# Optimization experiments

Hardware: AMD Instinct MI355X
Metric: run time of the kernel (lower is better)

Reference implementation:

```python
import jax, jax.numpy as jnp
import numpy as np

B, S, HID = 1, 2048, 2048
NH, NKV, D = 32, 4, 128   # query heads, kv heads, head_dim
ROPE_THETA = 1e6
EPS = 1e-6


def _rms_norm(x, w):
    # per-head RMSNorm over head_dim, computed in fp32 (Qwen3MoeRMSNorm)
    xf = x.astype(jnp.float32)
    var = jnp.mean(xf * xf, axis=-1, keepdims=True)
    return (w * (xf * jax.lax.rsqrt(var + EPS))).astype(x.dtype)


def _rotate_half(x):
    x1, x2 = jnp.split(x, 2, axis=-1)
    return jnp.concatenate([-x2, x1], axis=-1)


def setup_inputs() -> dict:
    key = jax.random.key(0)
    ks = jax.random.split(key, 5)
    hidden_states = jax.random.normal(ks[0], (B, S, HID), jnp.float32)
    # weights stored as (in, out); torch Linear computes x @ W.T with W (out,in) -- same math
    wq = jax.random.normal(ks[1], (HID, NH * D), jnp.float32) * 0.02
    wk = jax.random.normal(ks[2], (HID, NKV * D), jnp.float32) * 0.02
    wv = jax.random.normal(ks[3], (HID, NKV * D), jnp.float32) * 0.02
    wo = jax.random.normal(ks[4], (NH * D, HID), jnp.float32) * 0.02
    q_norm_w = jnp.ones((D,), jnp.float32)
    k_norm_w = jnp.ones((D,), jnp.float32)
    # RoPE tables (rotate_half convention, like HF Qwen3)
    inv_freq = 1.0 / (ROPE_THETA ** (jnp.arange(0, D, 2, dtype=jnp.float32) / D))
    freqs = jnp.arange(S, dtype=jnp.float32)[:, None] * inv_freq[None, :]  # [S, D/2]
    emb = jnp.concatenate([freqs, freqs], axis=-1)  # [S, D]
    cos, sin = jnp.cos(emb), jnp.sin(emb)
    # causal mask (True = keep)
    attention_mask = jnp.tril(jnp.ones((S, S), bool))[None, None]
    return {
        'hidden_states': hidden_states, 'cos': cos, 'sin': sin,
        'wq': wq, 'wk': wk, 'wv': wv, 'wo': wo,
        'q_norm_w': q_norm_w, 'k_norm_w': k_norm_w,
        'attention_mask': attention_mask, 'start_pos': 0,
    }


def reference(hidden_states, cos, sin, wq, wk, wv, wo, q_norm_w, k_norm_w,
              attention_mask, start_pos):
    b, s, _ = hidden_states.shape
    # projections + per-head RMSNorm, then [B, H, S, D]
    q = _rms_norm((hidden_states @ wq).reshape(b, s, NH, D), q_norm_w).transpose(0, 2, 1, 3)
    k = _rms_norm((hidden_states @ wk).reshape(b, s, NKV, D), k_norm_w).transpose(0, 2, 1, 3)
    v = (hidden_states @ wv).reshape(b, s, NKV, D).transpose(0, 2, 1, 3)
    # rotary embedding (rotate_half form); start_pos=0 -> tables already aligned
    c = cos[None, None, :, :]
    sn = sin[None, None, :, :]
    q = q * c + _rotate_half(q) * sn
    k = k * c + _rotate_half(k) * sn
    # GQA: repeat kv heads to match query heads
    groups = NH // NKV
    k = jnp.repeat(k, groups, axis=1)
    v = jnp.repeat(v, groups, axis=1)
    scaling = D ** -0.5
    scores = jnp.einsum('bhqd,bhkd->bhqk', q, k) * scaling  # [B, NH, S, S]
    scores = jnp.where(attention_mask, scores, jnp.float32(-1e9))
    attn = jax.nn.softmax(scores, axis=-1)
    out = jnp.einsum('bhqk,bhkd->bhqd', attn, v)  # [B, NH, S, D]
    out = out.transpose(0, 2, 1, 3).reshape(b, s, NH * D)
    return out @ wo
```

## Files before the change

### kernel.cpp

```cpp
#include <hip/hip_runtime.h>
#include <hip/hip_bf16.h>

using short4v = __attribute__((ext_vector_type(4))) short;
using short8 = __attribute__((ext_vector_type(8))) short;
using f32x4  = __attribute__((ext_vector_type(4))) float;

#define SEQ 2048
#define NHEAD 32
#define NKVH 4
#define HDIM 128
#define QK_SCALE_LOG2 (0.08838834764831845f * 1.44269504088896340f)

__device__ __forceinline__ float fast_exp2(float x) { return __builtin_amdgcn_exp2f(x); }
__device__ __forceinline__ float b2f(short u) {
    return __uint_as_float(((unsigned)(unsigned short)u) << 16);
}
__device__ __forceinline__ short f2bb(float f) {
    __hip_bfloat16 h = __float2bfloat16(f);
    return *reinterpret_cast<short*>(&h);
}

__global__ __launch_bounds__(256) void prep_kernel(
    const float* __restrict__ hs, __hip_bfloat16* __restrict__ hsb,
    const float* __restrict__ wq, const float* __restrict__ wk, const float* __restrict__ wv,
    const float* __restrict__ wo,
    __hip_bfloat16* __restrict__ WqkvT, __hip_bfloat16* __restrict__ WoT) {
    const int b = blockIdx.x, tid = threadIdx.x;
    if (b < 4096) {
        int i = b * 256 + tid;
        float4 v = ((const float4*)hs)[i];
        __hip_bfloat16 h4[4] = {__float2bfloat16(v.x), __float2bfloat16(v.y),
                                __float2bfloat16(v.z), __float2bfloat16(v.w)};
        ((ushort4*)hsb)[i] = *(ushort4*)h4;
        return;
    }
    __shared__ float tile[32][33];
    const float* W; __hip_bfloat16* Wt; int N, ld, nb, kb;
    if (b < 12288)      { int bb = b - 4096;  W = wq; Wt = WqkvT;                       N = 4096; ld = 2048; nb = (bb & 127) * 32; kb = (bb >> 7) * 32; }
    else if (b < 13312) { int bb = b - 12288; W = wk; Wt = WqkvT + (size_t)4096 * 2048; N = 512;  ld = 2048; nb = (bb & 15) * 32;  kb = (bb >> 4) * 32; }
    else if (b < 14336) { int bb = b - 13312; W = wv; Wt = WqkvT + (size_t)4608 * 2048; N = 512;  ld = 2048; nb = (bb & 15) * 32;  kb = (bb >> 4) * 32; }
    else                { int bb = b - 14336; W = wo; Wt = WoT;                         N = 2048; ld = 4096; nb = (bb & 63) * 32;  kb = (bb >> 6) * 32; }
    int tx = tid & 31, ty = tid >> 5;
    for (int j = 0; j < 32; j += 8)
        tile[ty + j][tx] = W[(size_t)(kb + ty + j) * N + nb + tx];
    __syncthreads();
    for (int j = 0; j < 32; j += 8)
        Wt[(size_t)(nb + ty + j) * ld + kb + tx] = __float2bfloat16(tile[tx][ty + j]);
}

__global__ void add2b_kernel(const __hip_bfloat16* __restrict__ a, const __hip_bfloat16* __restrict__ b,
                             float* __restrict__ o, int n4) {
    int i = blockIdx.x * blockDim.x + threadIdx.x;
    if (i >= n4) return;
    short4v x = ((const short4v*)a)[i];
    short4v y = ((const short4v*)b)[i];
    float4 z = {b2f(x[0]) + b2f(y[0]), b2f(x[1]) + b2f(y[1]),
                b2f(x[2]) + b2f(y[2]), b2f(x[3]) + b2f(y[3])};
    ((float4*)o)[i] = z;
}

#define BM 128
#define BN 128
#define BKK 32
template <typename OutT>
__global__ __launch_bounds__(256) void gemm_bt_kernel(
    const __hip_bfloat16* __restrict__ A, const __hip_bfloat16* __restrict__ Bt,
    OutT* __restrict__ C, int M, int N, int Kext, int ld, int koff, long long czstride) {
    A  += (size_t)blockIdx.z * koff;
    Bt += (size_t)blockIdx.z * koff;
    C  += (size_t)blockIdx.z * czstride;
    __shared__ __align__(16) __hip_bfloat16 sA[BM * BKK];
    __shared__ __align__(16) __hip_bfloat16 sB[BN * BKK];
    const int tid = threadIdx.x;
    const int w = tid >> 6, l = tid & 63;
    const int wr = w >> 1, wc = w & 1;
    const int row0 = blockIdx.y * BM;
    const int col0 = blockIdx.x * BN;
    const int srow = l >> 2;
    const int scol = (l & 3) * 8;

    f32x4 acc[4][4] = {};
    const int fr = l & 15;
    const int fc = (l >> 4) * 8;

    for (int k0 = 0; k0 < Kext; k0 += BKK) {
        for (int i = 0; i < 2; ++i) {
            int c = i * 4 + w;
            const __hip_bfloat16* ga = A + (size_t)(row0 + c * 16 + srow) * ld + k0 + scol;
            __builtin_amdgcn_global_load_lds((const __attribute__((address_space(1))) void*)ga,
                                             (__attribute__((address_space(3))) void*)&sA[c * 16 * BKK], 16, 0, 0);
            const __hip_bfloat16* gb = Bt + (size_t)(col0 + c * 16 + srow) * ld + k0 + scol;
            __builtin_amdgcn_global_load_lds((const __attribute__((address_space(1))) void*)gb,
                                             (__attribute__((address_space(3))) void*)&sB[c * 16 * BKK], 16, 0, 0);
        }
        __syncthreads();
        short8 af[4], bfr[4];
        for (int m = 0; m < 4; ++m)
            af[m] = *(const short8*)&sA[(wr * 64 + m * 16 + fr) * BKK + fc];
        for (int n = 0; n < 4; ++n)
            bfr[n] = *(const short8*)&sB[(wc * 64 + n * 16 + fr) * BKK + fc];
        for (int m = 0; m < 4; ++m)
            for (int n = 0; n < 4; ++n)
                acc[m][n] = __builtin_amdgcn_mfma_f32_16x16x32_bf16(af[m], bfr[n], acc[m][n], 0, 0, 0);
        __syncthreads();
    }
    const int fq = l >> 4;
    for (int m = 0; m < 4; ++m)
        for (int n = 0; n < 4; ++n)
            for (int r = 0; r < 4; ++r) {
                int row = row0 + wr * 64 + m * 16 + fq * 4 + r;
                int col = col0 + wc * 64 + n * 16 + fr;
                float v = acc[m][n][r];
                if constexpr (__is_same(OutT, float)) C[(size_t)row * N + col] = v;
                else C[(size_t)row * N + col] = __float2bfloat16(v);
            }
}

__global__ __launch_bounds__(256) void pack_kernel(
    const __hip_bfloat16* __restrict__ P0, const __hip_bfloat16* __restrict__ P1,
    const float* __restrict__ cosp, const float* __restrict__ sinp,
    const float* __restrict__ qnw, const float* __restrict__ knw,
    __hip_bfloat16* __restrict__ Qh, __hip_bfloat16* __restrict__ Kh, __hip_bfloat16* __restrict__ Vt) {
    const int tid = threadIdx.x;
    const int rloc = tid >> 4, l16 = tid & 15;
    const int r = blockIdx.y * 16 + rloc;
    const int s = blockIdx.x * 2 + (r >= 40 ? 1 : 0);
    const int slot = (r >= 40) ? r - 40 : r;
    int off;
    if (slot < 32)      off = slot * 128;
    else if (slot < 36) off = 4096 + (slot - 32) * 128;
    else                off = 4608 + (slot - 36) * 128;
    const int d0 = l16 * 4;
    const size_t base = (size_t)s * 5120 + off;

    short4v a0 = *(const short4v*)&P0[base + d0];
    short4v a1 = *(const short4v*)&P0[base + d0 + 64];
    short4v b0 = *(const short4v*)&P1[base + d0];
    short4v b1 = *(const short4v*)&P1[base + d0 + 64];
    float x1[4], x2[4];
    for (int j = 0; j < 4; ++j) {
        x1[j] = b2f(a0[j]) + b2f(b0[j]);
        x2[j] = b2f(a1[j]) + b2f(b1[j]);
    }

    if (slot >= 36) {
        int t = slot - 36;
        for (int j = 0; j < 4; ++j) {
            Vt[((size_t)t * 128 + d0 + j) * SEQ + s]      = __float2bfloat16(x1[j]);
            Vt[((size_t)t * 128 + d0 + 64 + j) * SEQ + s] = __float2bfloat16(x2[j]);
        }
        return;
    }
    float ss = 0.f;
    for (int j = 0; j < 4; ++j) ss += x1[j] * x1[j] + x2[j] * x2[j];
    for (int x = 1; x < 16; x <<= 1) ss += __shfl_xor(ss, x);
    float rs = rsqrtf(ss * (1.0f / 128.0f) + 1e-6f);

    f32x4 c4 = *(const f32x4*)&cosp[(size_t)s * 128 + d0];
    f32x4 s4 = *(const f32x4*)&sinp[(size_t)s * 128 + d0];
    const float* wgt = (slot < 32) ? qnw : knw;
    f32x4 w1 = *(const f32x4*)&wgt[d0];
    f32x4 w2 = *(const f32x4*)&wgt[d0 + 64];
    const float scl = (slot < 32) ? QK_SCALE_LOG2 : 1.0f;

    short4v o1, o2;
    for (int j = 0; j < 4; ++j) {
        float a = x1[j] * rs * w1[j], b = x2[j] * rs * w2[j];
        o1[j] = f2bb((a * c4[j] - b * s4[j]) * scl);
        o2[j] = f2bb((b * c4[j] + a * s4[j]) * scl);
    }
    __hip_bfloat16* dst;
    if (slot < 32) dst = Qh + ((size_t)slot * SEQ + s) * 128;
    else           dst = Kh + ((size_t)(slot - 32) * SEQ + s) * 128;
    *(short4v*)&dst[d0]      = o1;
    *(short4v*)&dst[d0 + 64] = o2;
}

__global__ __launch_bounds__(256, 2) void attn_kernel(
    const __hip_bfloat16* __restrict__ Qh,
    const __hip_bfloat16* __restrict__ Kh,
    const __hip_bfloat16* __restrict__ Vt,
    __hip_bfloat16* __restrict__ Oa) {
    __shared__ __align__(16) __hip_bfloat16 sK[2][64 * 128];
    __shared__ __align__(16) __hip_bfloat16 sV[2][128 * 64];
    __shared__ __align__(16) __hip_bfloat16 sP[4][16 * 72];

    const int tid = threadIdx.x;
    const int w = tid >> 6, l = tid & 63;
    const int bx = blockIdx.x;
    const int y = bx & 7;
    const int qt = 127 - (bx >> 3);
    const int qbase = qt * 16;
    const int hkv = y >> 1;
    const int h = y * 4 + w;
    const int fr = l & 15, g = l >> 4;

    const __hip_bfloat16* Qp = Qh + ((size_t)h * SEQ + qbase) * HDIM;
    const __hip_bfloat16* Kp = Kh + (size_t)hkv * SEQ * HDIM;
    const __hip_bfloat16* Vp = Vt + (size_t)hkv * HDIM * SEQ;
    __hip_bfloat16* myP = &sP[w][0];

    short8 qf[4];
    for (int c = 0; c < 4; ++c)
        qf[c] = *(const short8*)&Qp[fr * HDIM + c * 32 + g * 8];

    f32x4 oacc[8] = {};
    float mrow[4], lpart[4];
    for (int r = 0; r < 4; ++r) { mrow[r] = -3.0e38f; lpart[r] = 0.f; }

    const int xr = (fr & 7) << 4;
    const int ntiles = ((qbase + 15) >> 6) + 1;

    auto stage = [&](int buf, int kbase) {
        for (int i = 0; i < 4; ++i) {
            int blk = i * 4 + w;
            {
                int row = blk * 4 + (l >> 4);
                int cb = ((l & 15) * 16) ^ ((row & 7) << 4);
                const __hip_bfloat16* src = Kp + (size_t)(kbase + row) * HDIM + (cb >> 1);
                __builtin_amdgcn_global_load_lds((const __attribute__((address_space(1))) void*)src,
                    (__attribute__((address_space(3))) void*)&sK[buf][blk * 512], 16, 0, 0);
            }
            {
                int row = blk * 8 + (l >> 3);
                int cb = ((l & 7) * 16) ^ ((row & 7) << 4);
                const __hip_bfloat16* src = Vp + (size_t)row * SEQ + kbase + (cb >> 1);
                __builtin_amdgcn_global_load_lds((const __attribute__((address_space(1))) void*)src,
                    (__attribute__((address_space(3))) void*)&sV[buf][blk * 512], 16, 0, 0);
            }
        }
    };

    stage(0, 0);
    __syncthreads();

    for (int t = 0; t < ntiles; ++t) {
        const int kbase = t * 64;
        const int buf = t & 1;
        if (t + 1 < ntiles) stage(buf ^ 1, kbase + 64);

        f32x4 s[4] = {};
        __builtin_amdgcn_s_setprio(1);
        for (int j = 0; j < 4; ++j) {
            const __hip_bfloat16* kp = &sK[buf][(j * 16 + fr) * 128];
            for (int c = 0; c < 4; ++c) {
                short8 kf = *(const short8*)&kp[((c * 64 + g * 16) ^ xr) >> 1];
                s[j] = __builtin_amdgcn_mfma_f32_16x16x32_bf16(qf[c], kf, s[j], 0, 0, 0);
            }
        }
        __builtin_amdgcn_s_setprio(0);
        float v[4][4], mloc[4];
        const bool full = (kbase + 63 <= qbase);
        for (int r = 0; r < 4; ++r) {
            if (full) {
                v[r][0] = s[0][r]; v[r][1] = s[1][r]; v[r][2] = s[2][r]; v[r][3] = s[3][r];
            } else {
                const int qg = qbase + g * 4 + r;
                v[r][0] = (kbase + fr      <= qg) ? s[0][r] : -1e30f;
                v[r][1] = (kbase + 16 + fr <= qg) ? s[1][r] : -1e30f;
                v[r][2] = (kbase + 32 + fr <= qg) ? s[2][r] : -1e30f;
                v[r][3] = (kbase + 48 + fr <= qg) ? s[3][r] : -1e30f;
            }
            float m = fmaxf(fmaxf(v[r][0], v[r][1]), fmaxf(v[r][2], v[r][3]));
            for (int x = 1; x < 16; x <<= 1) m = fmaxf(m, __shfl_xor(m, x));
            mloc[r] = m;
        }
        int grow = (mloc[0] > mrow[0] + 12.0f) | (mloc[1] > mrow[1] + 12.0f) |
                   (mloc[2] > mrow[2] + 12.0f) | (mloc[3] > mrow[3] + 12.0f);
        if (__any(grow)) {
            for (int r = 0; r < 4; ++r) {
                float mnew = fmaxf(mrow[r], mloc[r]);
                float corr = fast_exp2(mrow[r] - mnew);
                mrow[r] = mnew;
                lpart[r] *= corr;
                for (int dt = 0; dt < 8; ++dt) oacc[dt][r] *= corr;
            }
        }
        for (int r = 0; r < 4; ++r) {
            float e0 = fast_exp2(v[r][0] - mrow[r]);
            float e1 = fast_exp2(v[r][1] - mrow[r]);
            float e2 = fast_exp2(v[r][2] - mrow[r]);
            float e3 = fast_exp2(v[r][3] - mrow[r]);
            lpart[r] += (e0 + e1) + (e2 + e3);
            const int prow = (g * 4 + r) * 72;
            myP[prow + fr]      = __float2bfloat16(e0);
            myP[prow + 16 + fr] = __float2bfloat16(e1);
            myP[prow + 32 + fr] = __float2bfloat16(e2);
            myP[prow + 48 + fr] = __float2bfloat16(e3);
        }
        short8 pa0 = *(const short8*)&myP[fr * 72 + g * 8];
        short8 pa1 = *(const short8*)&myP[fr * 72 + 32 + g * 8];
        __builtin_amdgcn_s_setprio(1);
        for (int dt = 0; dt < 8; ++dt) {
            const __hip_bfloat16* vp = &sV[buf][(dt * 16 + fr) * 64];
            short8 vb0 = *(const short8*)&vp[((g * 16)      ^ xr) >> 1];
            short8 vb1 = *(const short8*)&vp[((g * 16 + 64) ^ xr) >> 1];
            oacc[dt] = __builtin_amdgcn_mfma_f32_16x16x32_bf16(pa0, vb0, oacc[dt], 0, 0, 0);
            oacc[dt] = __builtin_amdgcn_mfma_f32_16x16x32_bf16(pa1, vb1, oacc[dt], 0, 0, 0);
        }
        __builtin_amdgcn_s_setprio(0);
        __syncthreads();
    }

    float inv[4];
    for (int r = 0; r < 4; ++r) {
        float lsum = lpart[r];
        for (int x = 1; x < 16; x <<= 1) lsum += __shfl_xor(lsum, x);
        inv[r] = 1.0f / lsum;
    }
    for (int dt = 0; dt < 8; ++dt)
        for (int r = 0; r < 4; ++r) {
            int qg = qbase + g * 4 + r;
            Oa[(size_t)qg * (NHEAD * HDIM) + h * HDIM + dt * 16 + fr] =
                __float2bfloat16(oacc[dt][r] * inv[r]);
        }
}

extern "C" void kernel_launch(void* const* d_in, const int* in_sizes, int n_in,
                              void* d_out, int out_size, void* d_ws, size_t ws_size,
                              hipStream_t stream) {
    const float* hs   = (const float*)d_in[0];
    const float* cosp = (const float*)d_in[1];
    const float* sinp = (const float*)d_in[2];
    const float* wq   = (const float*)d_in[3];
    const float* wk   = (const float*)d_in[4];
    const float* wv   = (const float*)d_in[5];
    const float* wo   = (const float*)d_in[6];
    const float* qnw  = (const float*)d_in[7];
    const float* knw  = (const float*)d_in[8];
    float* out = (float*)d_out;
    char* ws = (char*)d_ws;

    __hip_bfloat16* hsb    = (__hip_bfloat16*)(ws);
    __hip_bfloat16* WqkvT  = (__hip_bfloat16*)(ws + 8388608);
    __hip_bfloat16* WoT    = (__hip_bfloat16*)(ws + 29360128);
    __hip_bfloat16* P0     = (__hip_bfloat16*)(ws + 46137344);
    __hip_bfloat16* P1     = (__hip_bfloat16*)(ws + 67108864);
    __hip_bfloat16* Qh     = (__hip_bfloat16*)(ws + 8388608);
    __hip_bfloat16* Kh     = (__hip_bfloat16*)(ws + 25165824);
    __hip_bfloat16* Vt     = (__hip_bfloat16*)(ws + 27262976);
    __hip_bfloat16* Oa     = (__hip_bfloat16*)(ws + 46137344);
    __hip_bfloat16* Qb0    = (__hip_bfloat16*)(ws + 67108864);
    __hip_bfloat16* Qb1    = (__hip_bfloat16*)(ws + 75497472);

    prep_kernel<<<22528, 256, 0, stream>>>(hs, hsb, wq, wk, wv, wo, WqkvT, WoT);
    gemm_bt_kernel<__hip_bfloat16><<<dim3(40, 16, 2), 256, 0, stream>>>(
        hsb, WqkvT, P0, 2048, 5120, 1024, 2048, 1024, 10485760LL);
    pack_kernel<<<dim3(1024, 5), 256, 0, stream>>>(P0, P1, cosp, sinp, qnw, knw, Qh, Kh, Vt);
    attn_kernel<<<dim3(1024), 256, 0, stream>>>(Qh, Kh, Vt, Oa);
    gemm_bt_kernel<__hip_bfloat16><<<dim3(16, 16, 2), 256, 0, stream>>>(
        Oa, WoT, Qb0, 2048, 2048, 2048, 4096, 2048, 4194304LL);
    add2b_kernel<<<4096, 256, 0, stream>>>(Qb0, Qb1, out, (2048 * 2048) / 4);
}
```

Measured before the change: 245.0 us.

## Single-buffer attention KV via register prefetch and use 3-way split-K output GEMM

Attention now prefetches the next K/V tile into registers and writes it into a single LDS buffer after compute, replacing double-buffered direct-to-LDS loads. This halves K/V LDS use so occupancy can rise to 3 blocks per CU, at the cost of extra registers and a second barrier per tile. The output projection is split over three K chunks instead of two to give more blocks, with a 3-way add kernel to reduce the partial sums.

New measurement: 262.0 us. 7.0% more time.

```diff
diff --git a/kernel.cpp b/kernel.cpp
--- a/kernel.cpp
+++ b/kernel.cpp
@@ -48,15 +48,16 @@
         Wt[(size_t)(nb + ty + j) * ld + kb + tx] = __float2bfloat16(tile[tx][ty + j]);
 }
 
-__global__ void add2b_kernel(const __hip_bfloat16* __restrict__ a, const __hip_bfloat16* __restrict__ b,
-                             float* __restrict__ o, int n4) {
+__global__ void add3b_kernel(const __hip_bfloat16* __restrict__ a, const __hip_bfloat16* __restrict__ b,
+                             const __hip_bfloat16* __restrict__ c, float* __restrict__ o, int n4) {
     int i = blockIdx.x * blockDim.x + threadIdx.x;
     if (i >= n4) return;
     short4v x = ((const short4v*)a)[i];
     short4v y = ((const short4v*)b)[i];
-    float4 z = {b2f(x[0]) + b2f(y[0]), b2f(x[1]) + b2f(y[1]),
-                b2f(x[2]) + b2f(y[2]), b2f(x[3]) + b2f(y[3])};
-    ((float4*)o)[i] = z;
+    short4v z = ((const short4v*)c)[i];
+    float4 r = {b2f(x[0]) + b2f(y[0]) + b2f(z[0]), b2f(x[1]) + b2f(y[1]) + b2f(z[1]),
+                b2f(x[2]) + b2f(y[2]) + b2f(z[2]), b2f(x[3]) + b2f(y[3]) + b2f(z[3])};
+    ((float4*)o)[i] = r;
 }
 
 #define BM 128
@@ -65,9 +66,11 @@
 template <typename OutT>
 __global__ __launch_bounds__(256) void gemm_bt_kernel(
     const __hip_bfloat16* __restrict__ A, const __hip_bfloat16* __restrict__ Bt,
-    OutT* __restrict__ C, int M, int N, int Kext, int ld, int koff, long long czstride) {
-    A  += (size_t)blockIdx.z * koff;
-    Bt += (size_t)blockIdx.z * koff;
+    OutT* __restrict__ C, int M, int N, int KextMax, int ld, int koff, long long czstride, int Ktot) {
+    const int kstart = blockIdx.z * koff;
+    const int Kext = min(KextMax, Ktot - kstart);
+    A  += (size_t)kstart;
+    Bt += (size_t)kstart;
     C  += (size_t)blockIdx.z * czstride;
     __shared__ __align__(16) __hip_bfloat16 sA[BM * BKK];
     __shared__ __align__(16) __hip_bfloat16 sB[BN * BKK];
@@ -176,13 +179,13 @@
     *(short4v*)&dst[d0 + 64] = o2;
 }
 
-__global__ __launch_bounds__(256, 2) void attn_kernel(
+__global__ __launch_bounds__(256, 3) void attn_kernel(
     const __hip_bfloat16* __restrict__ Qh,
     const __hip_bfloat16* __restrict__ Kh,
     const __hip_bfloat16* __restrict__ Vt,
     __hip_bfloat16* __restrict__ Oa) {
-    __shared__ __align__(16) __hip_bfloat16 sK[2][64 * 128];
-    __shared__ __align__(16) __hip_bfloat16 sV[2][128 * 64];
+    __shared__ __align__(16) __hip_bfloat16 sK[64 * 128];
+    __shared__ __align__(16) __hip_bfloat16 sV[128 * 64];
     __shared__ __align__(16) __hip_bfloat16 sP[4][16 * 72];
 
     const int tid = threadIdx.x;
@@ -211,38 +214,39 @@
     const int xr = (fr & 7) << 4;
     const int ntiles = ((qbase + 15) >> 6) + 1;
 
-    auto stage = [&](int buf, int kbase) {
+    f32x4 kreg[4], vreg[4];
+    auto loadKV = [&](int kbase) {
         for (int i = 0; i < 4; ++i) {
-            int blk = i * 4 + w;
-            {
-                int row = blk * 4 + (l >> 4);
-                int cb = ((l & 15) * 16) ^ ((row & 7) << 4);
-                const __hip_bfloat16* src = Kp + (size_t)(kbase + row) * HDIM + (cb >> 1);
-                __builtin_amdgcn_global_load_lds((const __attribute__((address_space(1))) void*)src,
-                    (__attribute__((address_space(3))) void*)&sK[buf][blk * 512], 16, 0, 0);
-            }
-            {
-                int row = blk * 8 + (l >> 3);
-                int cb = ((l & 7) * 16) ^ ((row & 7) << 4);
-                const __hip_bfloat16* src = Vp + (size_t)row * SEQ + kbase + (cb >> 1);
-                __builtin_amdgcn_global_load_lds((const __attribute__((address_space(1))) void*)src,
-                    (__attribute__((address_space(3))) void*)&sV[buf][blk * 512], 16, 0, 0);
-            }
+            int ch = i * 256 + tid;
+            int rk = ch >> 4, ck = ch & 15;
+            kreg[i] = *(const f32x4*)&Kp[(size_t)(kbase + rk) * HDIM + ck * 8];
+            int rv = ch >> 3, cv = ch & 7;
+            vreg[i] = *(const f32x4*)&Vp[(size_t)rv * SEQ + kbase + cv * 8];
         }
     };
-
-    stage(0, 0);
+    auto writeKV = [&]() {
+        for (int i = 0; i < 4; ++i) {
+            int ch = i * 256 + tid;
+            int rk = ch >> 4, ck = ch & 15;
+            *(f32x4*)((char*)sK + rk * 256 + ((ck * 16) ^ ((rk & 7) << 4))) = kreg[i];
+            int rv = ch >> 3, cv = ch & 7;
+            *(f32x4*)((char*)sV + rv * 128 + ((cv * 16) ^ ((rv & 7) << 4))) = vreg[i];
+        }
+    };
+
+    loadKV(0);
+    writeKV();
     __syncthreads();
 
     for (int t = 0; t < ntiles; ++t) {
         const int kbase = t * 64;
-        const int buf = t & 1;
-        if (t + 1 < ntiles) stage(buf ^ 1, kbase + 64);
+        const bool more = (t + 1 < ntiles);
+        if (more) loadKV(kbase + 64);
 
         f32x4 s[4] = {};
         __builtin_amdgcn_s_setprio(1);
         for (int j = 0; j < 4; ++j) {
-            const __hip_bfloat16* kp = &sK[buf][(j * 16 + fr) * 128];
+            const __hip_bfloat16* kp = &sK[(j * 16 + fr) * 128];
             for (int c = 0; c < 4; ++c) {
                 short8 kf = *(const short8*)&kp[((c * 64 + g * 16) ^ xr) >> 1];
                 s[j] = __builtin_amdgcn_mfma_f32_16x16x32_bf16(qf[c], kf, s[j], 0, 0, 0);
@@ -292,7 +296,7 @@
         short8 pa1 = *(const short8*)&myP[fr * 72 + 32 + g * 8];
         __builtin_amdgcn_s_setprio(1);
         for (int dt = 0; dt < 8; ++dt) {
-            const __hip_bfloat16* vp = &sV[buf][(dt * 16 + fr) * 64];
+            const __hip_bfloat16* vp = &sV[(dt * 16 + fr) * 64];
             short8 vb0 = *(const short8*)&vp[((g * 16)      ^ xr) >> 1];
             short8 vb1 = *(const short8*)&vp[((g * 16 + 64) ^ xr) >> 1];
             oacc[dt] = __builtin_amdgcn_mfma_f32_16x16x32_bf16(pa0, vb0, oacc[dt], 0, 0, 0);
@@ -300,6 +304,10 @@
         }
         __builtin_amdgcn_s_setprio(0);
         __syncthreads();
+        if (more) {
+            writeKV();
+            __syncthreads();
+        }
     }
 
     float inv[4];
@@ -340,15 +348,14 @@
     __hip_bfloat16* Kh     = (__hip_bfloat16*)(ws + 25165824);
     __hip_bfloat16* Vt     = (__hip_bfloat16*)(ws + 27262976);
     __hip_bfloat16* Oa     = (__hip_bfloat16*)(ws + 46137344);
-    __hip_bfloat16* Qb0    = (__hip_bfloat16*)(ws + 67108864);
-    __hip_bfloat16* Qb1    = (__hip_bfloat16*)(ws + 75497472);
+    __hip_bfloat16* Qb     = (__hip_bfloat16*)(ws);
 
     prep_kernel<<<22528, 256, 0, stream>>>(hs, hsb, wq, wk, wv, wo, WqkvT, WoT);
     gemm_bt_kernel<__hip_bfloat16><<<dim3(40, 16, 2), 256, 0, stream>>>(
-        hsb, WqkvT, P0, 2048, 5120, 1024, 2048, 1024, 10485760LL);
+        hsb, WqkvT, P0, 2048, 5120, 1024, 2048, 1024, 10485760LL, 2048);
     pack_kernel<<<dim3(1024, 5), 256, 0, stream>>>(P0, P1, cosp, sinp, qnw, knw, Qh, Kh, Vt);
     attn_kernel<<<dim3(1024), 256, 0, stream>>>(Qh, Kh, Vt, Oa);
-    gemm_bt_kernel<__hip_bfloat16><<<dim3(16, 16, 2), 256, 0, stream>>>(
-        Oa, WoT, Qb0, 2048, 2048, 2048, 4096, 2048, 4194304LL);
-    add2b_kernel<<<4096, 256, 0, stream>>>(Qb0, Qb1, out, (2048 * 2048) / 4);
-}
+    gemm_bt_kernel<__hip_bfloat16><<<dim3(16, 16, 3), 256, 0, stream>>>(
+        Oa, WoT, Qb, 2048, 2048, 1376, 4096, 1376, 4194304LL, 4096);
+    add3b_kernel<<<4096, 256, 0, stream>>>(Qb, Qb + 4194304, Qb + 8388608, out, (2048 * 2048) / 4);
+}
```

## Pair causal query tiles per attention block and split Wo GEMM K three ways

Applied to the files above, without the earlier changes.

The attention kernel now processes two query tiles per block, a short one (qt) and its mirror (127-qt), sharing the staged K/V tiles so each block does balanced causal work and K/V loads are reused. The grid halves to 512 blocks, and register use roughly doubles for the accumulators. The output projection GEMM switches from a 2-way to a 3-way split-K with a ragged final chunk, and a new 3-input add kernel reduces the partials. This adds more parallel blocks for the GEMM at the cost of extra partial traffic.

Measured after the change: 241.2 us. About the same (-1.5%).

```diff
diff --git a/kernel.cpp b/kernel.cpp
--- a/kernel.cpp
+++ b/kernel.cpp
@@ -48,15 +48,16 @@
         Wt[(size_t)(nb + ty + j) * ld + kb + tx] = __float2bfloat16(tile[tx][ty + j]);
 }
 
-__global__ void add2b_kernel(const __hip_bfloat16* __restrict__ a, const __hip_bfloat16* __restrict__ b,
-                             float* __restrict__ o, int n4) {
+__global__ void add3b_kernel(const __hip_bfloat16* __restrict__ a, const __hip_bfloat16* __restrict__ b,
+                             const __hip_bfloat16* __restrict__ c, float* __restrict__ o, int n4) {
     int i = blockIdx.x * blockDim.x + threadIdx.x;
     if (i >= n4) return;
     short4v x = ((const short4v*)a)[i];
     short4v y = ((const short4v*)b)[i];
-    float4 z = {b2f(x[0]) + b2f(y[0]), b2f(x[1]) + b2f(y[1]),
-                b2f(x[2]) + b2f(y[2]), b2f(x[3]) + b2f(y[3])};
-    ((float4*)o)[i] = z;
+    short4v z = ((const short4v*)c)[i];
+    float4 r = {b2f(x[0]) + b2f(y[0]) + b2f(z[0]), b2f(x[1]) + b2f(y[1]) + b2f(z[1]),
+                b2f(x[2]) + b2f(y[2]) + b2f(z[2]), b2f(x[3]) + b2f(y[3]) + b2f(z[3])};
+    ((float4*)o)[i] = r;
 }
 
 #define BM 128
@@ -65,9 +66,11 @@
 template <typename OutT>
 __global__ __launch_bounds__(256) void gemm_bt_kernel(
     const __hip_bfloat16* __restrict__ A, const __hip_bfloat16* __restrict__ Bt,
-    OutT* __restrict__ C, int M, int N, int Kext, int ld, int koff, long long czstride) {
-    A  += (size_t)blockIdx.z * koff;
-    Bt += (size_t)blockIdx.z * koff;
+    OutT* __restrict__ C, int M, int N, int KextMax, int ld, int koff, long long czstride, int Ktot) {
+    const int kstart = blockIdx.z * koff;
+    const int Kext = min(KextMax, Ktot - kstart);
+    A  += (size_t)kstart;
+    Bt += (size_t)kstart;
     C  += (size_t)blockIdx.z * czstride;
     __shared__ __align__(16) __hip_bfloat16 sA[BM * BKK];
     __shared__ __align__(16) __hip_bfloat16 sB[BN * BKK];
@@ -189,27 +192,37 @@
     const int w = tid >> 6, l = tid & 63;
     const int bx = blockIdx.x;
     const int y = bx & 7;
-    const int qt = 127 - (bx >> 3);
-    const int qbase = qt * 16;
+    const int qtA = bx >> 3;
+    const int qbaseA = qtA * 16;
+    const int qbaseB = (127 - qtA) * 16;
     const int hkv = y >> 1;
     const int h = y * 4 + w;
     const int fr = l & 15, g = l >> 4;
 
-    const __hip_bfloat16* Qp = Qh + ((size_t)h * SEQ + qbase) * HDIM;
     const __hip_bfloat16* Kp = Kh + (size_t)hkv * SEQ * HDIM;
     const __hip_bfloat16* Vp = Vt + (size_t)hkv * HDIM * SEQ;
     __hip_bfloat16* myP = &sP[w][0];
 
-    short8 qf[4];
-    for (int c = 0; c < 4; ++c)
-        qf[c] = *(const short8*)&Qp[fr * HDIM + c * 32 + g * 8];
-
-    f32x4 oacc[8] = {};
-    float mrow[4], lpart[4];
-    for (int r = 0; r < 4; ++r) { mrow[r] = -3.0e38f; lpart[r] = 0.f; }
+    short8 qfA[4], qfB[4];
+    {
+        const __hip_bfloat16* QpA = Qh + ((size_t)h * SEQ + qbaseA) * HDIM;
+        const __hip_bfloat16* QpB = Qh + ((size_t)h * SEQ + qbaseB) * HDIM;
+        for (int c = 0; c < 4; ++c) {
+            qfA[c] = *(const short8*)&QpA[fr * HDIM + c * 32 + g * 8];
+            qfB[c] = *(const short8*)&QpB[fr * HDIM + c * 32 + g * 8];
+        }
+    }
+
+    f32x4 oaccA[8] = {}, oaccB[8] = {};
+    float mrowA[4], lpartA[4], mrowB[4], lpartB[4];
+    for (int r = 0; r < 4; ++r) {
+        mrowA[r] = -3.0e38f; lpartA[r] = 0.f;
+        mrowB[r] = -3.0e38f; lpartB[r] = 0.f;
+    }
 
     const int xr = (fr & 7) << 4;
-    const int ntiles = ((qbase + 15) >> 6) + 1;
+    const int nA = ((qbaseA + 15) >> 6) + 1;
+    const int nB = ((qbaseB + 15) >> 6) + 1;
 
     auto stage = [&](int buf, int kbase) {
         for (int i = 0; i < 4; ++i) {
@@ -231,88 +244,100 @@
         }
     };
 
+#define PROCESS(QF, OACC, MROW, LPART, QBASE)                                          \
+    {                                                                                  \
+        f32x4 s[4] = {};                                                               \
+        __builtin_amdgcn_s_setprio(1);                                                 \
+        for (int j = 0; j < 4; ++j) {                                                  \
+            const __hip_bfloat16* kp = &sK[buf][(j * 16 + fr) * 128];                  \
+            for (int c = 0; c < 4; ++c) {                                              \
+                short8 kf = *(const short8*)&kp[((c * 64 + g * 16) ^ xr) >> 1];        \
+                s[j] = __builtin_amdgcn_mfma_f32_16x16x32_bf16(QF[c], kf, s[j], 0, 0, 0); \
+            }                                                                          \
+        }                                                                              \
+        __builtin_amdgcn_s_setprio(0);                                                 \
+        float v[4][4], mloc[4];                                                        \
+        const bool full = (kbase + 63 <= (QBASE));                                     \
+        for (int r = 0; r < 4; ++r) {                                                  \
+            if (full) {                                                                \
+                v[r][0] = s[0][r]; v[r][1] = s[1][r]; v[r][2] = s[2][r]; v[r][3] = s[3][r]; \
+            } else {                                                                   \
+                const int qg = (QBASE) + g * 4 + r;                                    \
+                v[r][0] = (kbase + fr      <= qg) ? s[0][r] : -1e30f;                  \
+                v[r][1] = (kbase + 16 + fr <= qg) ? s[1][r] : -1e30f;                  \
+                v[r][2] = (kbase + 32 + fr <= qg) ? s[2][r] : -1e30f;                  \
+                v[r][3] = (kbase + 48 + fr <= qg) ? s[3][r] : -1e30f;                  \
+            }                                                                          \
+            float m = fmaxf(fmaxf(v[r][0], v[r][1]), fmaxf(v[r][2], v[r][3]));         \
+            for (int x = 1; x < 16; x <<= 1) m = fmaxf(m, __shfl_xor(m, x));           \
+            mloc[r] = m;                                                               \
+        }                                                                              \
+        int grow = (mloc[0] > MROW[0] + 12.0f) | (mloc[1] > MROW[1] + 12.0f) |         \
+                   (mloc[2] > MROW[2] + 12.0f) | (mloc[3] > MROW[3] + 12.0f);          \
+        if (__any(grow)) {                                                             \
+            for (int r = 0; r < 4; ++r) {                                              \
+                float mnew = fmaxf(MROW[r], mloc[r]);                                  \
+                float corr = fast_exp2(MROW[r] - mnew);                                \
+                MROW[r] = mnew;                                                        \
+                LPART[r] *= corr;                                                      \
+                for (int dt = 0; dt < 8; ++dt) OACC[dt][r] *= corr;                    \
+            }                                                                          \
+        }                                                                              \
+        for (int r = 0; r < 4; ++r) {                                                  \
+            float e0 = fast_exp2(v[r][0] - MROW[r]);                                   \
+            float e1 = fast_exp2(v[r][1] - MROW[r]);                                   \
+            float e2 = fast_exp2(v[r][2] - MROW[r]);                                   \
+            float e3 = fast_exp2(v[r][3] - MROW[r]);                                   \
+            LPART[r] += (e0 + e1) + (e2 + e3);                                         \
+            const int prow = (g * 4 + r) * 72;                                         \
+            myP[prow + fr]      = __float2bfloat16(e0);                                \
+            myP[prow + 16 + fr] = __float2bfloat16(e1);                                \
+            myP[prow + 32 + fr] = __float2bfloat16(e2);                                \
+            myP[prow + 48 + fr] = __float2bfloat16(e3);                                \
+        }                                                                              \
+        short8 pa0 = *(const short8*)&myP[fr * 72 + g * 8];                            \
+        short8 pa1 = *(const short8*)&myP[fr * 72 + 32 + g * 8];                       \
+        __builtin_amdgcn_s_setprio(1);                                                 \
+        for (int dt = 0; dt < 8; ++dt) {                                               \
+            const __hip_bfloat16* vp = &sV[buf][(dt * 16 + fr) * 64];                  \
+            short8 vb0 = *(const short8*)&vp[((g * 16)      ^ xr) >> 1];               \
+            short8 vb1 = *(const short8*)&vp[((g * 16 + 64) ^ xr) >> 1];               \
+            OACC[dt] = __builtin_amdgcn_mfma_f32_16x16x32_bf16(pa0, vb0, OACC[dt], 0, 0, 0); \
+            OACC[dt] = __builtin_amdgcn_mfma_f32_16x16x32_bf16(pa1, vb1, OACC[dt], 0, 0, 0); \
+        }                                                                              \
+        __builtin_amdgcn_s_setprio(0);                                                 \
+    }
+
     stage(0, 0);
     __syncthreads();
 
-    for (int t = 0; t < ntiles; ++t) {
+    for (int t = 0; t < nB; ++t) {
         const int kbase = t * 64;
         const int buf = t & 1;
-        if (t + 1 < ntiles) stage(buf ^ 1, kbase + 64);
-
-        f32x4 s[4] = {};
-        __builtin_amdgcn_s_setprio(1);
-        for (int j = 0; j < 4; ++j) {
-            const __hip_bfloat16* kp = &sK[buf][(j * 16 + fr) * 128];
-            for (int c = 0; c < 4; ++c) {
-                short8 kf = *(const short8*)&kp[((c * 64 + g * 16) ^ xr) >> 1];
-                s[j] = __builtin_amdgcn_mfma_f32_16x16x32_bf16(qf[c], kf, s[j], 0, 0, 0);
-            }
-        }
-        __builtin_amdgcn_s_setprio(0);
-        float v[4][4], mloc[4];
-        const bool full = (kbase + 63 <= qbase);
-        for (int r = 0; r < 4; ++r) {
-            if (full) {
-                v[r][0] = s[0][r]; v[r][1] = s[1][r]; v[r][2] = s[2][r]; v[r][3] = s[3][r];
-            } else {
-                const int qg = qbase + g * 4 + r;
-                v[r][0] = (kbase + fr      <= qg) ? s[0][r] : -1e30f;
-                v[r][1] = (kbase + 16 + fr <= qg) ? s[1][r] : -1e30f;
-                v[r][2] = (kbase + 32 + fr <= qg) ? s[2][r] : -1e30f;
-                v[r][3] = (kbase + 48 + fr <= qg) ? s[3][r] : -1e30f;
-            }
-            float m = fmaxf(fmaxf(v[r][0], v[r][1]), fmaxf(v[r][2], v[r][3]));
-            for (int x = 1; x < 16; x <<= 1) m = fmaxf(m, __shfl_xor(m, x));
-            mloc[r] = m;
-        }
-        int grow = (mloc[0] > mrow[0] + 12.0f) | (mloc[1] > mrow[1] + 12.0f) |
-                   (mloc[2] > mrow[2] + 12.0f) | (mloc[3] > mrow[3] + 12.0f);
-        if (__any(grow)) {
-            for (int r = 0; r < 4; ++r) {
-                float mnew = fmaxf(mrow[r], mloc[r]);
-                float corr = fast_exp2(mrow[r] - mnew);
-                mrow[r] = mnew;
-                lpart[r] *= corr;
-                for (int dt = 0; dt < 8; ++dt) oacc[dt][r] *= corr;
-            }
-        }
-        for (int r = 0; r < 4; ++r) {
-            float e0 = fast_exp2(v[r][0] - mrow[r]);
-            float e1 = fast_exp2(v[r][1] - mrow[r]);
-            float e2 = fast_exp2(v[r][2] - mrow[r]);
-            float e3 = fast_exp2(v[r][3] - mrow[r]);
-            lpart[r] += (e0 + e1) + (e2 + e3);
-            const int prow = (g * 4 + r) * 72;
-            myP[prow + fr]      = __float2bfloat16(e0);
-            myP[prow + 16 + fr] = __float2bfloat16(e1);
-            myP[prow + 32 + fr] = __float2bfloat16(e2);
-            myP[prow + 48 + fr] = __float2bfloat16(e3);
-        }
-        short8 pa0 = *(const short8*)&myP[fr * 72 + g * 8];
-        short8 pa1 = *(const short8*)&myP[fr * 72 + 32 + g * 8];
-        __builtin_amdgcn_s_setprio(1);
-        for (int dt = 0; dt < 8; ++dt) {
-            const __hip_bfloat16* vp = &sV[buf][(dt * 16 + fr) * 64];
-            short8 vb0 = *(const short8*)&vp[((g * 16)      ^ xr) >> 1];
-            short8 vb1 = *(const short8*)&vp[((g * 16 + 64) ^ xr) >> 1];
-            oacc[dt] = __builtin_amdgcn_mfma_f32_16x16x32_bf16(pa0, vb0, oacc[dt], 0, 0, 0);
-            oacc[dt] = __builtin_amdgcn_mfma_f32_16x16x32_bf16(pa1, vb1, oacc[dt], 0, 0, 0);
-        }
-        __builtin_amdgcn_s_setprio(0);
+        if (t + 1 < nB) stage(buf ^ 1, kbase + 64);
+
+        if (t < nA) PROCESS(qfA, oaccA, mrowA, lpartA, qbaseA);
+        PROCESS(qfB, oaccB, mrowB, lpartB, qbaseB);
+
         __syncthreads();
     }
-
-    float inv[4];
+#undef PROCESS
+
+    float invA[4], invB[4];
     for (int r = 0; r < 4; ++r) {
-        float lsum = lpart[r];
-        for (int x = 1; x < 16; x <<= 1) lsum += __shfl_xor(lsum, x);
-        inv[r] = 1.0f / lsum;
+        float la = lpartA[r], lb = lpartB[r];
+        for (int x = 1; x < 16; x <<= 1) { la += __shfl_xor(la, x); lb += __shfl_xor(lb, x); }
+        invA[r] = 1.0f / la;
+        invB[r] = 1.0f / lb;
     }
     for (int dt = 0; dt < 8; ++dt)
         for (int r = 0; r < 4; ++r) {
-            int qg = qbase + g * 4 + r;
-            Oa[(size_t)qg * (NHEAD * HDIM) + h * HDIM + dt * 16 + fr] =
-                __float2bfloat16(oacc[dt][r] * inv[r]);
+            int qgA = qbaseA + g * 4 + r;
+            int qgB = qbaseB + g * 4 + r;
+            Oa[(size_t)qgA * (NHEAD * HDIM) + h * HDIM + dt * 16 + fr] =
+                __float2bfloat16(oaccA[dt][r] * invA[r]);
+            Oa[(size_t)qgB * (NHEAD * HDIM) + h * HDIM + dt * 16 + fr] =
+                __float2bfloat16(oaccB[dt][r] * invB[r]);
         }
 }
 
@@ -340,15 +365,14 @@
     __hip_bfloat16* Kh     = (__hip_bfloat16*)(ws + 25165824);
     __hip_bfloat16* Vt     = (__hip_bfloat16*)(ws + 27262976);
     __hip_bfloat16* Oa     = (__hip_bfloat16*)(ws + 46137344);
-    __hip_bfloat16* Qb0    = (__hip_bfloat16*)(ws + 67108864);
-    __hip_bfloat16* Qb1    = (__hip_bfloat16*)(ws + 75497472);
+    __hip_bfloat16* Qb     = (__hip_bfloat16*)(ws);
 
     prep_kernel<<<22528, 256, 0, stream>>>(hs, hsb, wq, wk, wv, wo, WqkvT, WoT);
     gemm_bt_kernel<__hip_bfloat16><<<dim3(40, 16, 2), 256, 0, stream>>>(
-        hsb, WqkvT, P0, 2048, 5120, 1024, 2048, 1024, 10485760LL);
+        hsb, WqkvT, P0, 2048, 5120, 1024, 2048, 1024, 10485760LL, 2048);
     pack_kernel<<<dim3(1024, 5), 256, 0, stream>>>(P0, P1, cosp, sinp, qnw, knw, Qh, Kh, Vt);
-    attn_kernel<<<dim3(1024), 256, 0, stream>>>(Qh, Kh, Vt, Oa);
-    gemm_bt_kernel<__hip_bfloat16><<<dim3(16, 16, 2), 256, 0, stream>>>(
-        Oa, WoT, Qb0, 2048, 2048, 2048, 4096, 2048, 4194304LL);
-    add2b_kernel<<<4096, 256, 0, stream>>>(Qb0, Qb1, out, (2048 * 2048) / 4);
-}
+    attn_kernel<<<dim3(512), 256, 0, stream>>>(Qh, Kh, Vt, Oa);
+    gemm_bt_kernel<__hip_bfloat16><<<dim3(16, 16, 3), 256, 0, stream>>>(
+        Oa, WoT, Qb, 2048, 2048, 1376, 4096, 1376, 4194304LL, 4096);
+    add3b_kernel<<<4096, 256, 0, stream>>>(Qb, Qb + 4194304, Qb + 8388608, out, (2048 * 2048) / 4);
+}
```

## Transpose attention S tile for per-lane softmax and split O-proj into three K slices

Applied to the files above, without the earlier changes.

The attention kernel swaps the MFMA operand order so each lane holds one query row's scores. Row max and sum then need only two cross-group shuffles instead of four 16-lane reductions per row, and P is written as packed 4-element vectors. Separately, the output projection is split-K over three slices instead of two (768 blocks instead of 512) with a three-way bf16 add at the end, to improve CU occupancy. The cost is more partial-sum traffic and an uneven final K slice, and the Qb workspace now aliases hsb at offset zero.

Result: faster. 223.4 us (-8.8%).

```diff
diff --git a/kernel.cpp b/kernel.cpp
--- a/kernel.cpp
+++ b/kernel.cpp
@@ -48,15 +48,16 @@
         Wt[(size_t)(nb + ty + j) * ld + kb + tx] = __float2bfloat16(tile[tx][ty + j]);
 }
 
-__global__ void add2b_kernel(const __hip_bfloat16* __restrict__ a, const __hip_bfloat16* __restrict__ b,
-                             float* __restrict__ o, int n4) {
+__global__ void add3b_kernel(const __hip_bfloat16* __restrict__ a, const __hip_bfloat16* __restrict__ b,
+                             const __hip_bfloat16* __restrict__ c, float* __restrict__ o, int n4) {
     int i = blockIdx.x * blockDim.x + threadIdx.x;
     if (i >= n4) return;
     short4v x = ((const short4v*)a)[i];
     short4v y = ((const short4v*)b)[i];
-    float4 z = {b2f(x[0]) + b2f(y[0]), b2f(x[1]) + b2f(y[1]),
-                b2f(x[2]) + b2f(y[2]), b2f(x[3]) + b2f(y[3])};
-    ((float4*)o)[i] = z;
+    short4v z = ((const short4v*)c)[i];
+    float4 r = {b2f(x[0]) + b2f(y[0]) + b2f(z[0]), b2f(x[1]) + b2f(y[1]) + b2f(z[1]),
+                b2f(x[2]) + b2f(y[2]) + b2f(z[2]), b2f(x[3]) + b2f(y[3]) + b2f(z[3])};
+    ((float4*)o)[i] = r;
 }
 
 #define BM 128
@@ -65,9 +66,11 @@
 template <typename OutT>
 __global__ __launch_bounds__(256) void gemm_bt_kernel(
     const __hip_bfloat16* __restrict__ A, const __hip_bfloat16* __restrict__ Bt,
-    OutT* __restrict__ C, int M, int N, int Kext, int ld, int koff, long long czstride) {
-    A  += (size_t)blockIdx.z * koff;
-    Bt += (size_t)blockIdx.z * koff;
+    OutT* __restrict__ C, int M, int N, int KextMax, int ld, int koff, long long czstride, int Ktot) {
+    const int kstart = blockIdx.z * koff;
+    const int Kext = min(KextMax, Ktot - kstart);
+    A  += (size_t)kstart;
+    Bt += (size_t)kstart;
     C  += (size_t)blockIdx.z * czstride;
     __shared__ __align__(16) __hip_bfloat16 sA[BM * BKK];
     __shared__ __align__(16) __hip_bfloat16 sB[BN * BKK];
@@ -205,10 +208,11 @@
         qf[c] = *(const short8*)&Qp[fr * HDIM + c * 32 + g * 8];
 
     f32x4 oacc[8] = {};
-    float mrow[4], lpart[4];
-    for (int r = 0; r < 4; ++r) { mrow[r] = -3.0e38f; lpart[r] = 0.f; }
+    float m_s = -3.0e38f;
+    float l_s = 0.f;
 
     const int xr = (fr & 7) << 4;
+    const int qg = qbase + fr;
     const int ntiles = ((qbase + 15) >> 6) + 1;
 
     auto stage = [&](int buf, int kbase) {
@@ -245,48 +249,51 @@
             const __hip_bfloat16* kp = &sK[buf][(j * 16 + fr) * 128];
             for (int c = 0; c < 4; ++c) {
                 short8 kf = *(const short8*)&kp[((c * 64 + g * 16) ^ xr) >> 1];
-                s[j] = __builtin_amdgcn_mfma_f32_16x16x32_bf16(qf[c], kf, s[j], 0, 0, 0);
+                s[j] = __builtin_amdgcn_mfma_f32_16x16x32_bf16(kf, qf[c], s[j], 0, 0, 0);
             }
         }
         __builtin_amdgcn_s_setprio(0);
-        float v[4][4], mloc[4];
+
+        float v[4][4];
         const bool full = (kbase + 63 <= qbase);
-        for (int r = 0; r < 4; ++r) {
-            if (full) {
-                v[r][0] = s[0][r]; v[r][1] = s[1][r]; v[r][2] = s[2][r]; v[r][3] = s[3][r];
-            } else {
-                const int qg = qbase + g * 4 + r;
-                v[r][0] = (kbase + fr      <= qg) ? s[0][r] : -1e30f;
-                v[r][1] = (kbase + 16 + fr <= qg) ? s[1][r] : -1e30f;
-                v[r][2] = (kbase + 32 + fr <= qg) ? s[2][r] : -1e30f;
-                v[r][3] = (kbase + 48 + fr <= qg) ? s[3][r] : -1e30f;
-            }
-            float m = fmaxf(fmaxf(v[r][0], v[r][1]), fmaxf(v[r][2], v[r][3]));
-            for (int x = 1; x < 16; x <<= 1) m = fmaxf(m, __shfl_xor(m, x));
-            mloc[r] = m;
-        }
-        int grow = (mloc[0] > mrow[0] + 12.0f) | (mloc[1] > mrow[1] + 12.0f) |
-                   (mloc[2] > mrow[2] + 12.0f) | (mloc[3] > mrow[3] + 12.0f);
-        if (__any(grow)) {
-            for (int r = 0; r < 4; ++r) {
-                float mnew = fmaxf(mrow[r], mloc[r]);
-                float corr = fast_exp2(mrow[r] - mnew);
-                mrow[r] = mnew;
-                lpart[r] *= corr;
-                for (int dt = 0; dt < 8; ++dt) oacc[dt][r] *= corr;
-            }
-        }
-        for (int r = 0; r < 4; ++r) {
-            float e0 = fast_exp2(v[r][0] - mrow[r]);
-            float e1 = fast_exp2(v[r][1] - mrow[r]);
-            float e2 = fast_exp2(v[r][2] - mrow[r]);
-            float e3 = fast_exp2(v[r][3] - mrow[r]);
-            lpart[r] += (e0 + e1) + (e2 + e3);
-            const int prow = (g * 4 + r) * 72;
-            myP[prow + fr]      = __float2bfloat16(e0);
-            myP[prow + 16 + fr] = __float2bfloat16(e1);
-            myP[prow + 32 + fr] = __float2bfloat16(e2);
-            myP[prow + 48 + fr] = __float2bfloat16(e3);
+        if (full) {
+            for (int j = 0; j < 4; ++j)
+                for (int r = 0; r < 4; ++r) v[j][r] = s[j][r];
+        } else {
+            const int kb0 = kbase + g * 4;
+            for (int j = 0; j < 4; ++j)
+                for (int r = 0; r < 4; ++r)
+                    v[j][r] = (kb0 + j * 16 + r <= qg) ? s[j][r] : -1e30f;
+        }
+        float m0 = fmaxf(fmaxf(v[0][0], v[0][1]), fmaxf(v[0][2], v[0][3]));
+        float m1 = fmaxf(fmaxf(v[1][0], v[1][1]), fmaxf(v[1][2], v[1][3]));
+        float m2 = fmaxf(fmaxf(v[2][0], v[2][1]), fmaxf(v[2][2], v[2][3]));
+        float m3 = fmaxf(fmaxf(v[3][0], v[3][1]), fmaxf(v[3][2], v[3][3]));
+        float m = fmaxf(fmaxf(m0, m1), fmaxf(m2, m3));
+        m = fmaxf(m, __shfl_xor(m, 16));
+        m = fmaxf(m, __shfl_xor(m, 32));
+        if (__any(m > m_s + 12.0f)) {
+            float mnew = fmaxf(m_s, m);
+            float corr = fast_exp2(m_s - mnew);
+            m_s = mnew;
+            l_s *= corr;
+            float c0 = __shfl(corr, g * 4 + 0);
+            float c1 = __shfl(corr, g * 4 + 1);
+            float c2 = __shfl(corr, g * 4 + 2);
+            float c3 = __shfl(corr, g * 4 + 3);
+            for (int dt = 0; dt < 8; ++dt) {
+                oacc[dt][0] *= c0; oacc[dt][1] *= c1;
+                oacc[dt][2] *= c2; oacc[dt][3] *= c3;
+            }
+        }
+        for (int j = 0; j < 4; ++j) {
+            float e0 = fast_exp2(v[j][0] - m_s);
+            float e1 = fast_exp2(v[j][1] - m_s);
+            float e2 = fast_exp2(v[j][2] - m_s);
+            float e3 = fast_exp2(v[j][3] - m_s);
+            l_s += (e0 + e1) + (e2 + e3);
+            short4v pw = {f2bb(e0), f2bb(e1), f2bb(e2), f2bb(e3)};
+            *(short4v*)((char*)myP + fr * 144 + j * 32 + g * 8) = pw;
         }
         short8 pa0 = *(const short8*)&myP[fr * 72 + g * 8];
         short8 pa1 = *(const short8*)&myP[fr * 72 + 32 + g * 8];
@@ -302,16 +309,15 @@
         __syncthreads();
     }
 
+    l_s += __shfl_xor(l_s, 16);
+    l_s += __shfl_xor(l_s, 32);
     float inv[4];
-    for (int r = 0; r < 4; ++r) {
-        float lsum = lpart[r];
-        for (int x = 1; x < 16; x <<= 1) lsum += __shfl_xor(lsum, x);
-        inv[r] = 1.0f / lsum;
-    }
+    for (int r = 0; r < 4; ++r)
+        inv[r] = 1.0f / __shfl(l_s, g * 4 + r);
     for (int dt = 0; dt < 8; ++dt)
         for (int r = 0; r < 4; ++r) {
-            int qg = qbase + g * 4 + r;
-            Oa[(size_t)qg * (NHEAD * HDIM) + h * HDIM + dt * 16 + fr] =
+            int qq = qbase + g * 4 + r;
+            Oa[(size_t)qq * (NHEAD * HDIM) + h * HDIM + dt * 16 + fr] =
                 __float2bfloat16(oacc[dt][r] * inv[r]);
         }
 }
@@ -340,15 +346,14 @@
     __hip_bfloat16* Kh     = (__hip_bfloat16*)(ws + 25165824);
     __hip_bfloat16* Vt     = (__hip_bfloat16*)(ws + 27262976);
     __hip_bfloat16* Oa     = (__hip_bfloat16*)(ws + 46137344);
-    __hip_bfloat16* Qb0    = (__hip_bfloat16*)(ws + 67108864);
-    __hip_bfloat16* Qb1    = (__hip_bfloat16*)(ws + 75497472);
+    __hip_bfloat16* Qb     = (__hip_bfloat16*)(ws);
 
     prep_kernel<<<22528, 256, 0, stream>>>(hs, hsb, wq, wk, wv, wo, WqkvT, WoT);
     gemm_bt_kernel<__hip_bfloat16><<<dim3(40, 16, 2), 256, 0, stream>>>(
-        hsb, WqkvT, P0, 2048, 5120, 1024, 2048, 1024, 10485760LL);
+        hsb, WqkvT, P0, 2048, 5120, 1024, 2048, 1024, 10485760LL, 2048);
     pack_kernel<<<dim3(1024, 5), 256, 0, stream>>>(P0, P1, cosp, sinp, qnw, knw, Qh, Kh, Vt);
     attn_kernel<<<dim3(1024), 256, 0, stream>>>(Qh, Kh, Vt, Oa);
-    gemm_bt_kernel<__hip_bfloat16><<<dim3(16, 16, 2), 256, 0, stream>>>(
-        Oa, WoT, Qb0, 2048, 2048, 2048, 4096, 2048, 4194304LL);
-    add2b_kernel<<<4096, 256, 0, stream>>>(Qb0, Qb1, out, (2048 * 2048) / 4);
-}
+    gemm_bt_kernel<__hip_bfloat16><<<dim3(16, 16, 3), 256, 0, stream>>>(
+        Oa, WoT, Qb, 2048, 2048, 1376, 4096, 1376, 4194304LL, 4096);
+    add3b_kernel<<<4096, 256, 0, stream>>>(Qb, Qb + 4194304, Qb + 8388608, out, (2048 * 2048) / 4);
+}
```
